# Kernel optimization log

Measured on AMD Instinct MI355X. Metric: run time of the kernel, lower is better.

The kernel has to match this reference:

```python
import jax, jax.numpy as jnp
import numpy as np

B, D, NB = 2_000_000, 16, 64


def setup_inputs() -> dict:
    key = jax.random.key(0)
    k1, k2, k3, k4 = jax.random.split(key, 4)
    y_pred = jax.random.uniform(k1, (B, D), jnp.float32)
    y_true = jax.random.uniform(k2, (B, D), jnp.float32)
    conditional_info = jax.random.uniform(k3, (B,), jnp.float32)
    bin_weights = jax.random.uniform(k4, (NB,), jnp.float32)
    # bins_values dict (keys 1..NB) -> sorted edge array covering the data range
    bin_edges = jnp.linspace(0.0, 1.0, NB, dtype=jnp.float32)
    return {
        "y_pred": y_pred,
        "y_true": y_true,
        "bin_weights": bin_weights,
        "conditional_info": conditional_info,
        "bin_edges": bin_edges,
    }


def reference(y_pred, y_true, bin_weights, conditional_info, bin_edges):
    MIN_WEIGHT = 0.01
    EPS = 1e-7
    # Serial per-point bin search over sorted points == bucketize:
    # point with edges[i] < x < edges[i+1] (0-indexed) gets 1-indexed bin i+1;
    # points past the last edge fall in bin NB (the loop saturates there).
    bin_1idx = jnp.clip(
        jnp.searchsorted(bin_edges, conditional_info, side="left"),
        1, bin_edges.shape[0],
    )  # [B], values in 1..NB
    w = jnp.maximum(bin_weights[bin_1idx - 1], MIN_WEIGHT)  # [B]
    p = jnp.clip(y_pred, EPS, 1.0 - EPS)
    # F.binary_cross_entropy(p, y, weight=w[:, None]) -> mean of weighted elementwise BCE
    bce = -(y_true * jnp.log(p) + (1.0 - y_true) * jnp.log1p(-p))  # [B, D]
    return jnp.mean(w[:, None] * bce)
```

## Files before the change

### kernel.cpp

```cpp
#include <hip/hip_runtime.h>

#define NB_MAX 64
#define THREADS 256
#define MAX_BLOCKS 2048

__global__ __launch_bounds__(THREADS)
void wbce_partial_kernel(const float* __restrict__ y_pred,
                         const float* __restrict__ y_true,
                         const float* __restrict__ bin_weights,
                         const float* __restrict__ cond,
                         const float* __restrict__ bin_edges,
                         float* __restrict__ partials,
                         long long nq, int qshift, int nb)
{
    __shared__ float s_edges[NB_MAX];
    __shared__ float s_w[NB_MAX];
    int tid = threadIdx.x;
    if (tid < nb) {
        s_edges[tid] = bin_edges[tid];
        s_w[tid] = fmaxf(bin_weights[tid], 0.01f);
    }
    __syncthreads();

    const float4* __restrict__ yp4 = (const float4*)y_pred;
    const float4* __restrict__ yt4 = (const float4*)y_true;

    const float EPS = 1e-7f;
    const float PHI = 1.0f - 1e-7f;

    float acc = 0.0f;
    long long stride = (long long)gridDim.x * blockDim.x;
    for (long long q = (long long)blockIdx.x * blockDim.x + tid; q < nq; q += stride) {
        long long row = q >> qshift;
        float x = cond[row];

        int lo = 0, hi = nb;
        while (lo < hi) {
            int mid = (lo + hi) >> 1;
            if (s_edges[mid] < x) lo = mid + 1; else hi = mid;
        }
        int bin1 = lo < 1 ? 1 : (lo > nb ? nb : lo);
        float w = s_w[bin1 - 1];

        float4 p4 = yp4[q];
        float4 t4 = yt4[q];
        float s = 0.0f;
        #pragma unroll
        for (int j = 0; j < 4; ++j) {
            float p = ((const float*)&p4)[j];
            float t = ((const float*)&t4)[j];
            p = fminf(fmaxf(p, EPS), PHI);
            s += t * __logf(p) + (1.0f - t) * __logf(1.0f - p);
        }
        acc -= w * s;
    }

    #pragma unroll
    for (int off = 32; off > 0; off >>= 1)
        acc += __shfl_down(acc, off, 64);

    __shared__ float s_red[THREADS / 64];
    int wave = tid >> 6;
    int lane = tid & 63;
    if (lane == 0) s_red[wave] = acc;
    __syncthreads();
    if (tid == 0) {
        float b = 0.0f;
        #pragma unroll
        for (int w2 = 0; w2 < THREADS / 64; ++w2) b += s_red[w2];
        partials[blockIdx.x] = b;
    }
}

__global__ __launch_bounds__(THREADS)
void wbce_final_kernel(const float* __restrict__ partials, int n,
                       float* __restrict__ out, float inv_count)
{
    int tid = threadIdx.x;
    float acc = 0.0f;
    for (int i = tid; i < n; i += THREADS) acc += partials[i];

    #pragma unroll
    for (int off = 32; off > 0; off >>= 1)
        acc += __shfl_down(acc, off, 64);

    __shared__ float s_red[THREADS / 64];
    int wave = tid >> 6;
    int lane = tid & 63;
    if (lane == 0) s_red[wave] = acc;
    __syncthreads();
    if (tid == 0) {
        float b = 0.0f;
        #pragma unroll
        for (int w2 = 0; w2 < THREADS / 64; ++w2) b += s_red[w2];
        out[0] = b * inv_count;
    }
}

extern "C" void kernel_launch(void* const* d_in, const int* in_sizes, int n_in,
                              void* d_out, int out_size, void* d_ws, size_t ws_size,
                              hipStream_t stream) {
    const float* y_pred = (const float*)d_in[0];
    const float* y_true = (const float*)d_in[1];
    const float* bw     = (const float*)d_in[2];
    const float* cond   = (const float*)d_in[3];
    const float* edges  = (const float*)d_in[4];

    long long total = in_sizes[0];
    long long Bn    = in_sizes[3];
    int D  = (int)(total / Bn);
    int nb = in_sizes[2];

    long long nq  = total / 4;
    int qpr = D / 4;
    int qshift = 0;
    while ((1 << qshift) < qpr) qshift++;

    float* partials = (float*)d_ws;

    long long want = (nq + THREADS - 1) / THREADS;
    int grid = (int)(want < MAX_BLOCKS ? want : MAX_BLOCKS);
    if (grid < 1) grid = 1;

    wbce_partial_kernel<<<grid, THREADS, 0, stream>>>(
        y_pred, y_true, bw, cond, edges, partials, nq, qshift, nb);

    float inv = 1.0f / (float)total;
    wbce_final_kernel<<<1, THREADS, 0, stream>>>(partials, grid, (float*)d_out, inv);
}
```

Measured before the change: 51.74 us.

## Process one full row per thread to amortize bin search and weight lookup

Switches from one float4 per thread to one full row per thread, so the conditional load and binary search over bin edges happen once per row instead of once per float4. The BCE math is rewritten using log2 with a single ln2 scale, a med3 clamp, and the t*(lp-lq)+lq factorization. Per-thread strided row access makes each wave's loads span more cache lines, which may hurt coalescing in this bandwidth-bound kernel.

```diff
diff --git a/kernel.cpp b/kernel.cpp
--- a/kernel.cpp
+++ b/kernel.cpp
@@ -5,13 +5,13 @@
 #define MAX_BLOCKS 2048
 
 __global__ __launch_bounds__(THREADS)
-void wbce_partial_kernel(const float* __restrict__ y_pred,
-                         const float* __restrict__ y_true,
-                         const float* __restrict__ bin_weights,
-                         const float* __restrict__ cond,
-                         const float* __restrict__ bin_edges,
-                         float* __restrict__ partials,
-                         long long nq, int qshift, int nb)
+void wbce_row_kernel(const float* __restrict__ y_pred,
+                     const float* __restrict__ y_true,
+                     const float* __restrict__ bin_weights,
+                     const float* __restrict__ cond,
+                     const float* __restrict__ bin_edges,
+                     float* __restrict__ partials,
+                     long long nrows, int dqshift, int nb)
 {
     __shared__ float s_edges[NB_MAX];
     __shared__ float s_w[NB_MAX];
@@ -22,37 +22,44 @@
     }
     __syncthreads();
 
-    const float4* __restrict__ yp4 = (const float4*)y_pred;
-    const float4* __restrict__ yt4 = (const float4*)y_true;
-
     const float EPS = 1e-7f;
-    const float PHI = 1.0f - 1e-7f;
+    const float PHI = 0.99999994f;
+    const float LN2 = 0.6931471805599453f;
+    const int dq = 1 << dqshift;
 
     float acc = 0.0f;
     long long stride = (long long)gridDim.x * blockDim.x;
-    for (long long q = (long long)blockIdx.x * blockDim.x + tid; q < nq; q += stride) {
-        long long row = q >> qshift;
-        float x = cond[row];
+    for (long long r = (long long)blockIdx.x * blockDim.x + tid; r < nrows; r += stride) {
+        float x = cond[r];
 
         int lo = 0, hi = nb;
         while (lo < hi) {
             int mid = (lo + hi) >> 1;
             if (s_edges[mid] < x) lo = mid + 1; else hi = mid;
         }
-        int bin1 = lo < 1 ? 1 : (lo > nb ? nb : lo);
-        float w = s_w[bin1 - 1];
+        int b1 = lo < 1 ? 1 : (lo > nb ? nb : lo);
+        float w = s_w[b1 - 1];
 
-        float4 p4 = yp4[q];
-        float4 t4 = yt4[q];
-        float s = 0.0f;
-        #pragma unroll
-        for (int j = 0; j < 4; ++j) {
-            float p = ((const float*)&p4)[j];
-            float t = ((const float*)&t4)[j];
-            p = fminf(fmaxf(p, EPS), PHI);
-            s += t * __logf(p) + (1.0f - t) * __logf(1.0f - p);
+        const float4* __restrict__ yp4 = (const float4*)y_pred + (r << dqshift);
+        const float4* __restrict__ yt4 = (const float4*)y_true + (r << dqshift);
+
+        float sA = 0.0f, sB = 0.0f;
+        #pragma unroll 4
+        for (int j = 0; j < dq; ++j) {
+            float4 p4 = yp4[j];
+            float4 t4 = yt4[j];
+            #pragma unroll
+            for (int k = 0; k < 4; ++k) {
+                float p = ((const float*)&p4)[k];
+                float t = ((const float*)&t4)[k];
+                p = __builtin_amdgcn_fmed3f(p, EPS, PHI);
+                float lp = __log2f(p);
+                float lq = __log2f(1.0f - p);
+                sA += lq;
+                sB = fmaf(t, lp - lq, sB);
+            }
         }
-        acc -= w * s;
+        acc = fmaf(-w * LN2, sA + sB, acc);
     }
 
     #pragma unroll
@@ -111,19 +118,18 @@
     int D  = (int)(total / Bn);
     int nb = in_sizes[2];
 
-    long long nq  = total / 4;
-    int qpr = D / 4;
-    int qshift = 0;
-    while ((1 << qshift) < qpr) qshift++;
+    int dq = D / 4;
+    int dqshift = 0;
+    while ((1 << dqshift) < dq) dqshift++;
 
     float* partials = (float*)d_ws;
 
-    long long want = (nq + THREADS - 1) / THREADS;
+    long long want = (Bn + THREADS - 1) / THREADS;
     int grid = (int)(want < MAX_BLOCKS ? want : MAX_BLOCKS);
     if (grid < 1) grid = 1;
 
-    wbce_partial_kernel<<<grid, THREADS, 0, stream>>>(
-        y_pred, y_true, bw, cond, edges, partials, nq, qshift, nb);
+    wbce_row_kernel<<<grid, THREADS, 0, stream>>>(
+        y_pred, y_true, bw, cond, edges, partials, Bn, dqshift, nb);
 
     float inv = 1.0f / (float)total;
     wbce_final_kernel<<<1, THREADS, 0, stream>>>(partials, grid, (float*)d_out, inv);
```

Result: faster. 48.38 us (-6.5%).
